# Kernel optimization log

Measured on AMD Instinct MI355X. Metric: run time of the kernel, lower is better.

Reference implementation:

```python
import jax, jax.numpy as jnp
import numpy as np

N_NODES = 50000
N_EDGES = 200000
N_GRAPHS = 1024
D = 24          # node feature dim (fixed by Set2Set(24))
E_FEAT = 8
E_HID = 128


def setup_inputs() -> dict:
    key = jax.random.key(0)
    ks = jax.random.split(key, 20)
    s = 0.1  # weight scale for numerical sanity
    inp = {
        "x": jax.random.normal(ks[0], (N_NODES, D), jnp.float32),
        "edge_attr": jax.random.normal(ks[1], (N_EDGES, E_FEAT), jnp.float32),
        # edge-network MLP: E_FEAT -> E_HID -> D*D
        "w_e1": jax.random.normal(ks[2], (E_FEAT, E_HID), jnp.float32) * s,
        "b_e1": jnp.zeros((E_HID,), jnp.float32),
        "w_e2": jax.random.normal(ks[3], (E_HID, D * D), jnp.float32) * s,
        "b_e2": jnp.zeros((D * D,), jnp.float32),
        # NNConv root weight + bias
        "root": jax.random.normal(ks[4], (D, D), jnp.float32) * s,
        "bias_conv": jnp.zeros((D,), jnp.float32),
        # Set2Set LSTM (input 2D=48, hidden D=24), torch gate order i,f,g,o
        "w_ih": jax.random.normal(ks[5], (4 * D, 2 * D), jnp.float32) * s,
        "w_hh": jax.random.normal(ks[6], (4 * D, D), jnp.float32) * s,
        "b_ih": jnp.zeros((4 * D,), jnp.float32),
        "b_hh": jnp.zeros((4 * D,), jnp.float32),
        # heads
        "w_fc2": jax.random.normal(ks[7], (2 * D, 8), jnp.float32) * s,
        "b_fc2": jnp.zeros((8,), jnp.float32),
        "w_fc3": jax.random.normal(ks[8], (8, 2), jnp.float32) * s,
        "b_fc3": jnp.zeros((2,), jnp.float32),
        "edge_index": jax.random.randint(ks[9], (2, N_EDGES), 0, N_NODES, jnp.int64),
        "batch": jnp.sort(jax.random.randint(ks[10], (N_NODES,), 0, N_GRAPHS, jnp.int64)),
    }
    return inp


def _nnconv(x, edge_attr, edge_index, w_e1, b_e1, w_e2, b_e2, root, bias_conv):
    src, dst = edge_index[0], edge_index[1]
    h = jax.nn.relu(edge_attr @ w_e1 + b_e1)
    w = (h @ w_e2 + b_e2).reshape(-1, D, D)          # [E, D_in, D_out]
    msg = jnp.einsum('ei,eio->eo', x[src], w)         # gather + per-edge matvec
    s = jax.ops.segment_sum(msg, dst, num_segments=N_NODES)
    cnt = jax.ops.segment_sum(jnp.ones((msg.shape[0],), msg.dtype), dst, num_segments=N_NODES)
    agg = s / jnp.maximum(cnt, 1.0)[:, None]          # scatter-mean
    return agg + x @ root + bias_conv


def _set2set(x, batch, w_ih, w_hh, b_ih, b_hh):
    B = N_GRAPHS
    q_star = jnp.zeros((B, 2 * D), x.dtype)
    h = jnp.zeros((B, D), x.dtype)
    c = jnp.zeros((B, D), x.dtype)
    for _ in range(3):  # processing_steps=3 (fixed small loop)
        gates = q_star @ w_ih.T + b_ih + h @ w_hh.T + b_hh
        i, f, g, o = jnp.split(gates, 4, axis=-1)
        c = jax.nn.sigmoid(f) * c + jax.nn.sigmoid(i) * jnp.tanh(g)
        h = jax.nn.sigmoid(o) * jnp.tanh(c)
        q = h                                         # [B, D]
        e = jnp.sum(x * q[batch], axis=-1)            # [N]
        e_max = jax.ops.segment_max(e, batch, num_segments=B)
        e_max = jnp.where(jnp.isfinite(e_max), e_max, 0.0)
        ex = jnp.exp(e - e_max[batch])
        denom = jax.ops.segment_sum(ex, batch, num_segments=B)
        a = ex / jnp.maximum(denom, 1e-16)[batch]     # per-graph softmax
        r = jax.ops.segment_sum(a[:, None] * x, batch, num_segments=B)
        q_star = jnp.concatenate([q, r], axis=-1)
    return q_star


def reference(x, edge_attr, w_e1, b_e1, w_e2, b_e2, root, bias_conv,
              w_ih, w_hh, b_ih, b_hh, w_fc2, b_fc2, w_fc3, b_fc3,
              edge_index, batch):
    x = _nnconv(x, edge_attr, edge_index, w_e1, b_e1, w_e2, b_e2, root, bias_conv)
    x = jax.nn.relu(x)
    x = _nnconv(x, edge_attr, edge_index, w_e1, b_e1, w_e2, b_e2, root, bias_conv)
    q_star = _set2set(x, batch, w_ih, w_hh, b_ih, b_hh)
    out = jax.nn.relu(q_star @ w_fc2 + b_fc2)
    return out @ w_fc3 + b_fc3                        # [B, 2]
```

## Files before the change

kernel.cpp:

```cpp
#include <hip/hip_runtime.h>
#include <math.h>

#define N_NODES 50000
#define N_EDGES 200000
#define N_GRAPHS 1024
#define DIM 24
#define EF 8
#define EH 128
#define DD 576
#define HSTR 136

typedef __attribute__((ext_vector_type(8))) _Float16 f16x8;
typedef __attribute__((ext_vector_type(4))) _Float16 f16x4;
typedef __attribute__((ext_vector_type(2))) _Float16 f16x2;
typedef __attribute__((ext_vector_type(4))) float float4e;
typedef _Float16 f16;

static __device__ __forceinline__ float sigm(float x) { return 1.0f / (1.0f + expf(-x)); }

__global__ void deg_kernel(const int* __restrict__ dst, int* __restrict__ deg) {
    int i = blockIdx.x * blockDim.x + threadIdx.x;
    if (i < N_EDGES) atomicAdd(&deg[dst[i]], 1);
}

__global__ __launch_bounds__(256) void bz_kernel(const float* __restrict__ w2,
                                                 const float* __restrict__ b2,
                                                 f16* __restrict__ Bz) {
    int idx = blockIdx.x * 256 + threadIdx.x;
    if (idx >= 97 * 2 * 64 * 8) return;
    int kk = idx & 7, lane = (idx >> 3) & 63, nt = (idx >> 9) & 1, p = idx >> 10;
    int q = lane >> 4, l16 = lane & 15, n = nt * 16 + l16;
    float v = 0.0f;
    if (p < 96) {
        int si = p / 24, i = p % 24;
        int k = si * 32 + q * 8 + kk;
        if (n < 24) v = w2[(size_t)k * DD + i * 24 + n];
    } else {
        int i2 = q * 8 + kk;
        if (i2 < 24 && n < 24) v = b2[i2 * 24 + n];
    }
    Bz[idx] = (f16)v;
}

__global__ __launch_bounds__(256, 4) void conv_kernel(
    const float* __restrict__ x, const float* __restrict__ ea,
    const float* __restrict__ w1, const float* __restrict__ b1,
    const f16* __restrict__ Bz,
    const int* __restrict__ src, const int* __restrict__ dst,
    float* __restrict__ agg)
{
    __shared__ f16 hs[128 * HSTR];

    const int t  = threadIdx.x;
    const int e0 = blockIdx.x * 128;

    const int lane = t & 63;
    const int wave = t >> 6;
    const int l16  = lane & 15;
    const int quad = lane >> 4;
    const int ebase = e0 + wave * 32;

    f16x2 xa[12], xb[12];
    {
        int ega = ebase + l16;      if (ega >= N_EDGES) ega = N_EDGES - 1;
        int egb = ebase + 16 + l16; if (egb >= N_EDGES) egb = N_EDGES - 1;
        const float* xra = x + (size_t)src[ega] * DIM;
        const float* xrb = x + (size_t)src[egb] * DIM;
        #pragma unroll
        for (int j4 = 0; j4 < 6; ++j4) {
            float4 va = *(const float4*)(xra + j4 * 4);
            float4 vb = *(const float4*)(xrb + j4 * 4);
            xa[j4 * 2]     = (f16x2){(f16)va.x, (f16)va.y};
            xa[j4 * 2 + 1] = (f16x2){(f16)va.z, (f16)va.w};
            xb[j4 * 2]     = (f16x2){(f16)vb.x, (f16)vb.y};
            xb[j4 * 2 + 1] = (f16x2){(f16)vb.z, (f16)vb.w};
        }
    }

    {
        const int s5 = t & 31;
        const int eb = (t >> 5) * 16;
        float wv[EF][4];
        #pragma unroll
        for (int j = 0; j < EF; ++j) {
            float4 v = *(const float4*)(w1 + j * EH + s5 * 4);
            wv[j][0] = v.x; wv[j][1] = v.y; wv[j][2] = v.z; wv[j][3] = v.w;
        }
        float4 bv = *(const float4*)(b1 + s5 * 4);
        const float bvv[4] = {bv.x, bv.y, bv.z, bv.w};
        #pragma unroll
        for (int e = 0; e < 16; ++e) {
            int eg = e0 + eb + e; if (eg >= N_EDGES) eg = N_EDGES - 1;
            const float* ear = ea + (size_t)eg * EF;
            float4 a0 = *(const float4*)ear;
            float4 a1 = *(const float4*)(ear + 4);
            const float av[EF] = {a0.x, a0.y, a0.z, a0.w, a1.x, a1.y, a1.z, a1.w};
            float r[4] = {bvv[0], bvv[1], bvv[2], bvv[3]};
            #pragma unroll
            for (int j = 0; j < EF; ++j)
                #pragma unroll
                for (int c = 0; c < 4; ++c)
                    r[c] = fmaf(av[j], wv[j][c], r[c]);
            f16x4 hq = { (f16)fmaxf(r[0], 0.0f), (f16)fmaxf(r[1], 0.0f),
                         (f16)fmaxf(r[2], 0.0f), (f16)fmaxf(r[3], 0.0f) };
            *(f16x4*)&hs[(eb + e) * HSTR + s5 * 4] = hq;
        }
    }

    const f16x8* bz = (const f16x8*)Bz + lane;
    f16x8 pb0[2], pb1[2];
    pb0[0] = bz[0];   pb1[0] = bz[64];
    pb0[1] = bz[128]; pb1[1] = bz[192];

    __syncthreads();

    float4e a00 = {0.f,0.f,0.f,0.f}, a01 = {0.f,0.f,0.f,0.f};
    float4e a10 = {0.f,0.f,0.f,0.f}, a11 = {0.f,0.f,0.f,0.f};

    #pragma unroll
    for (int si = 0; si < 4; ++si) {
        union { f16x8 v; f16x2 p[4]; } h0u, h1u;
        h0u.v = *(const f16x8*)&hs[(wave * 32 + l16) * HSTR + si * 32 + quad * 8];
        h1u.v = *(const f16x8*)&hs[(wave * 32 + 16 + l16) * HSTR + si * 32 + quad * 8];
        #pragma unroll
        for (int i = 0; i < 24; ++i) {
            const int p = si * 24 + i;
            f16x8 b0 = pb0[p & 1], b1v = pb1[p & 1];
            if (p + 2 <= 96) {
                pb0[p & 1] = bz[(p + 2) * 128];
                pb1[p & 1] = bz[(p + 2) * 128 + 64];
            }
            f16 xea = (i & 1) ? xa[i >> 1][1] : xa[i >> 1][0];
            f16 xeb = (i & 1) ? xb[i >> 1][1] : xb[i >> 1][0];
            f16x2 xa2 = {xea, xea}, xb2 = {xeb, xeb};
            union { f16x8 v; f16x2 p[4]; } a0u, a1u;
            #pragma unroll
            for (int j = 0; j < 4; ++j) {
                a0u.p[j] = h0u.p[j] * xa2;
                a1u.p[j] = h1u.p[j] * xb2;
            }
            a00 = __builtin_amdgcn_mfma_f32_16x16x32_f16(a0u.v, b0,  a00, 0, 0, 0);
            a10 = __builtin_amdgcn_mfma_f32_16x16x32_f16(a1u.v, b0,  a10, 0, 0, 0);
            a01 = __builtin_amdgcn_mfma_f32_16x16x32_f16(a0u.v, b1v, a01, 0, 0, 0);
            a11 = __builtin_amdgcn_mfma_f32_16x16x32_f16(a1u.v, b1v, a11, 0, 0, 0);
            if ((p % 12) == 11) __syncthreads();
        }
    }

    {
        union { f16x8 v; f16x2 p[4]; } a0u, a1u;
        f16x2 z2 = {(f16)0.f, (f16)0.f};
        if (quad == 0)      { a0u.p[0]=xa[0]; a0u.p[1]=xa[1]; a0u.p[2]=xa[2];  a0u.p[3]=xa[3];
                              a1u.p[0]=xb[0]; a1u.p[1]=xb[1]; a1u.p[2]=xb[2];  a1u.p[3]=xb[3];  }
        else if (quad == 1) { a0u.p[0]=xa[4]; a0u.p[1]=xa[5]; a0u.p[2]=xa[6];  a0u.p[3]=xa[7];
                              a1u.p[0]=xb[4]; a1u.p[1]=xb[5]; a1u.p[2]=xb[6];  a1u.p[3]=xb[7];  }
        else if (quad == 2) { a0u.p[0]=xa[8]; a0u.p[1]=xa[9]; a0u.p[2]=xa[10]; a0u.p[3]=xa[11];
                              a1u.p[0]=xb[8]; a1u.p[1]=xb[9]; a1u.p[2]=xb[10]; a1u.p[3]=xb[11]; }
        else                { a0u.p[0]=z2; a0u.p[1]=z2; a0u.p[2]=z2; a0u.p[3]=z2;
                              a1u.p[0]=z2; a1u.p[1]=z2; a1u.p[2]=z2; a1u.p[3]=z2; }
        a00 = __builtin_amdgcn_mfma_f32_16x16x32_f16(a0u.v, pb0[0], a00, 0, 0, 0);
        a10 = __builtin_amdgcn_mfma_f32_16x16x32_f16(a1u.v, pb0[0], a10, 0, 0, 0);
        a01 = __builtin_amdgcn_mfma_f32_16x16x32_f16(a0u.v, pb1[0], a01, 0, 0, 0);
        a11 = __builtin_amdgcn_mfma_f32_16x16x32_f16(a1u.v, pb1[0], a11, 0, 0, 0);
    }

    #pragma unroll
    for (int r = 0; r < 4; ++r) {
        int er = ebase + quad * 4 + r;
        if (er < N_EDGES) {
            int d = dst[er];
            atomicAdd(&agg[(size_t)d * DIM + l16], a00[r]);
            if (l16 < 8) atomicAdd(&agg[(size_t)d * DIM + 16 + l16], a01[r]);
        }
        int er2 = ebase + 16 + quad * 4 + r;
        if (er2 < N_EDGES) {
            int d = dst[er2];
            atomicAdd(&agg[(size_t)d * DIM + l16], a10[r]);
            if (l16 < 8) atomicAdd(&agg[(size_t)d * DIM + 16 + l16], a11[r]);
        }
    }
}

__global__ void combine_kernel(
    const float* __restrict__ x_in, const float* __restrict__ agg,
    const int* __restrict__ deg, const float* __restrict__ root,
    const float* __restrict__ bias, float* __restrict__ x_out, int do_relu)
{
    int t = blockIdx.x * blockDim.x + threadIdx.x;
    if (t >= N_NODES * DIM) return;
    int v = t / DIM, o = t % DIM;
    int dg = deg[v];
    float d = dg > 0 ? (float)dg : 1.0f;
    float a = agg[t] / d + bias[o];
    const float* xr = x_in + (size_t)v * DIM;
    #pragma unroll
    for (int i = 0; i < DIM; ++i) a = fmaf(xr[i], root[i * DIM + o], a);
    x_out[t] = do_relu ? fmaxf(a, 0.0f) : a;
}

__global__ void lstm_kernel(
    const float* __restrict__ q_star, const float* __restrict__ h_in,
    const float* __restrict__ c_in, const float* __restrict__ w_ih,
    const float* __restrict__ w_hh, const float* __restrict__ b_ih,
    const float* __restrict__ b_hh, float* __restrict__ h_out,
    float* __restrict__ c_out)
{
    int t = blockIdx.x * blockDim.x + threadIdx.x;
    if (t >= N_GRAPHS * DIM) return;
    int g = t / DIM, d = t % DIM;
    const float* qs = q_star + (size_t)g * 48;
    const float* hv = h_in + (size_t)g * DIM;
    float gate[4];
    #pragma unroll
    for (int r4 = 0; r4 < 4; ++r4) {
        int r = r4 * DIM + d;
        float a = b_ih[r] + b_hh[r];
        const float* wi = w_ih + (size_t)r * 48;
        const float* wh = w_hh + (size_t)r * DIM;
        for (int j = 0; j < 48; ++j) a = fmaf(qs[j], wi[j], a);
        #pragma unroll
        for (int j = 0; j < DIM; ++j) a = fmaf(hv[j], wh[j], a);
        gate[r4] = a;
    }
    float c = sigm(gate[1]) * c_in[t] + sigm(gate[0]) * tanhf(gate[2]);
    h_out[t] = sigm(gate[3]) * tanhf(c);
    c_out[t] = c;
}

__global__ __launch_bounds__(64) void attn_kernel(
    const float* __restrict__ x, const int* __restrict__ batch,
    const float* __restrict__ h, float* __restrict__ q_star,
    float* __restrict__ e_buf)
{
    const int g = blockIdx.x;
    const int t = threadIdx.x;
    __shared__ int s_lo, s_hi;
    __shared__ float qs[DIM];
    if (t == 0) {
        int lo = 0, hi = N_NODES;
        while (lo < hi) { int m = (lo + hi) >> 1; if (batch[m] < g) lo = m + 1; else hi = m; }
        s_lo = lo;
        int lo2 = lo; hi = N_NODES;
        while (lo2 < hi) { int m = (lo2 + hi) >> 1; if (batch[m] <= g) lo2 = m + 1; else hi = m; }
        s_hi = lo2;
    }
    if (t < DIM) qs[t] = h[(size_t)g * DIM + t];
    __syncthreads();
    const int lo = s_lo, hi = s_hi;

    float mx = -INFINITY;
    for (int n = lo + t; n < hi; n += 64) {
        const float* xr = x + (size_t)n * DIM;
        float e = 0.0f;
        #pragma unroll
        for (int d = 0; d < DIM; ++d) e = fmaf(xr[d], qs[d], e);
        e_buf[n] = e;
        mx = fmaxf(mx, e);
    }
    #pragma unroll
    for (int off = 32; off; off >>= 1) mx = fmaxf(mx, __shfl_xor(mx, off));
    float m = (hi > lo) ? mx : 0.0f;

    float sum = 0.0f;
    for (int n = lo + t; n < hi; n += 64) sum += expf(e_buf[n] - m);
    #pragma unroll
    for (int off = 32; off; off >>= 1) sum += __shfl_xor(sum, off);
    float denom = fmaxf(sum, 1e-16f);

    float r[DIM];
    #pragma unroll
    for (int d = 0; d < DIM; ++d) r[d] = 0.0f;
    for (int n = lo + t; n < hi; n += 64) {
        float a = expf(e_buf[n] - m) / denom;
        const float* xr = x + (size_t)n * DIM;
        #pragma unroll
        for (int d = 0; d < DIM; ++d) r[d] = fmaf(a, xr[d], r[d]);
    }
    #pragma unroll
    for (int d = 0; d < DIM; ++d) {
        #pragma unroll
        for (int off = 32; off; off >>= 1) r[d] += __shfl_xor(r[d], off);
    }
    if (t < DIM) {
        q_star[(size_t)g * 48 + t] = qs[t];
        q_star[(size_t)g * 48 + DIM + t] = r[t];
    }
}

__global__ void head_kernel(
    const float* __restrict__ q_star, const float* __restrict__ w2,
    const float* __restrict__ b2, const float* __restrict__ w3,
    const float* __restrict__ b3, float* __restrict__ out)
{
    int g = blockIdx.x * blockDim.x + threadIdx.x;
    if (g >= N_GRAPHS) return;
    const float* q = q_star + (size_t)g * 48;
    float z[8];
    #pragma unroll
    for (int k = 0; k < 8; ++k) {
        float a = b2[k];
        for (int j = 0; j < 48; ++j) a = fmaf(q[j], w2[j * 8 + k], a);
        z[k] = fmaxf(a, 0.0f);
    }
    #pragma unroll
    for (int c = 0; c < 2; ++c) {
        float a = b3[c];
        #pragma unroll
        for (int k = 0; k < 8; ++k) a = fmaf(z[k], w3[k * 2 + c], a);
        out[(size_t)g * 2 + c] = a;
    }
}

extern "C" void kernel_launch(void* const* d_in, const int* in_sizes, int n_in,
                              void* d_out, int out_size, void* d_ws, size_t ws_size,
                              hipStream_t stream) {
    const float* x      = (const float*)d_in[0];
    const float* ea     = (const float*)d_in[1];
    const float* w_e1   = (const float*)d_in[2];
    const float* b_e1   = (const float*)d_in[3];
    const float* w_e2   = (const float*)d_in[4];
    const float* b_e2   = (const float*)d_in[5];
    const float* root   = (const float*)d_in[6];
    const float* bias_c = (const float*)d_in[7];
    const float* w_ih   = (const float*)d_in[8];
    const float* w_hh   = (const float*)d_in[9];
    const float* b_ih   = (const float*)d_in[10];
    const float* b_hh   = (const float*)d_in[11];
    const float* w_fc2  = (const float*)d_in[12];
    const float* b_fc2  = (const float*)d_in[13];
    const float* w_fc3  = (const float*)d_in[14];
    const float* b_fc3  = (const float*)d_in[15];
    const int*   eidx   = (const int*)d_in[16];
    const int*   batch  = (const int*)d_in[17];
    const int* esrc = eidx;
    const int* edst = eidx + N_EDGES;
    float* out = (float*)d_out;

    char* ws = (char*)d_ws;
    float* agg   = (float*)(ws);
    int*   deg   = (int*)  (ws + 4800000);
    float* qstar = (float*)(ws + 5000000);
    float* h0    = (float*)(ws + 5196608);
    float* c0    = h0 + 24576;
    float* h1    = c0 + 24576;
    float* c1    = h1 + 24576;
    float* ebuf  = (float*)(ws + 5589824);
    float* x1    = (float*)(ws + 5789824);
    float* x2    = (float*)(ws + 10589824);
    f16*   Bz    = (f16*)  (ws + 15389824);

    hipMemsetAsync(ws, 0, 5589824, stream);

    deg_kernel<<<(N_EDGES + 255) / 256, 256, 0, stream>>>(edst, deg);
    bz_kernel<<<(97 * 2 * 64 * 8 + 255) / 256, 256, 0, stream>>>(w_e2, b_e2, Bz);

    conv_kernel<<<(N_EDGES + 127) / 128, 256, 0, stream>>>(x, ea, w_e1, b_e1, Bz, esrc, edst, agg);
    combine_kernel<<<(N_NODES * DIM + 255) / 256, 256, 0, stream>>>(x, agg, deg, root, bias_c, x1, 1);

    hipMemsetAsync(agg, 0, 4800000, stream);
    conv_kernel<<<(N_EDGES + 127) / 128, 256, 0, stream>>>(x1, ea, w_e1, b_e1, Bz, esrc, edst, agg);
    combine_kernel<<<(N_NODES * DIM + 255) / 256, 256, 0, stream>>>(x1, agg, deg, root, bias_c, x2, 0);

    float *hA = h0, *cA = c0, *hB = h1, *cB = c1;
    for (int it = 0; it < 3; ++it) {
        lstm_kernel<<<(N_GRAPHS * DIM + 255) / 256, 256, 0, stream>>>(
            qstar, hA, cA, w_ih, w_hh, b_ih, b_hh, hB, cB);
        attn_kernel<<<N_GRAPHS, 64, 0, stream>>>(x2, batch, hB, qstar, ebuf);
        float* th = hA; hA = hB; hB = th;
        float* tc = cA; cA = cB; cB = tc;
    }

    head_kernel<<<(N_GRAPHS + 255) / 256, 256, 0, stream>>>(qstar, w_fc2, b_fc2, w_fc3, b_fc3, out);
}
```

Measured before the change: 330.2 us.

## Fuse Set2Set LSTM, attention iterations and head into one per-graph kernel

Replaces the three rounds of LSTM and attention launches plus the head kernel with a single kernel in which each block owns one graph and keeps h, c and q_star in shared memory across all iterations. The attention pass becomes a single-pass online softmax with vectorized float4 row loads, so the e buffer and the extra passes over x are gone. This removes seven launches and the global round trips for the intermediates. In exchange the LSTM gate math now runs per block with only 64 threads, and the online rescaling adds extra exp calls when the running max changes.

```diff
diff --git a/kernel.cpp b/kernel.cpp
--- a/kernel.cpp
+++ b/kernel.cpp
@@ -198,44 +198,20 @@
     x_out[t] = do_relu ? fmaxf(a, 0.0f) : a;
 }
 
-__global__ void lstm_kernel(
-    const float* __restrict__ q_star, const float* __restrict__ h_in,
-    const float* __restrict__ c_in, const float* __restrict__ w_ih,
-    const float* __restrict__ w_hh, const float* __restrict__ b_ih,
-    const float* __restrict__ b_hh, float* __restrict__ h_out,
-    float* __restrict__ c_out)
-{
-    int t = blockIdx.x * blockDim.x + threadIdx.x;
-    if (t >= N_GRAPHS * DIM) return;
-    int g = t / DIM, d = t % DIM;
-    const float* qs = q_star + (size_t)g * 48;
-    const float* hv = h_in + (size_t)g * DIM;
-    float gate[4];
-    #pragma unroll
-    for (int r4 = 0; r4 < 4; ++r4) {
-        int r = r4 * DIM + d;
-        float a = b_ih[r] + b_hh[r];
-        const float* wi = w_ih + (size_t)r * 48;
-        const float* wh = w_hh + (size_t)r * DIM;
-        for (int j = 0; j < 48; ++j) a = fmaf(qs[j], wi[j], a);
-        #pragma unroll
-        for (int j = 0; j < DIM; ++j) a = fmaf(hv[j], wh[j], a);
-        gate[r4] = a;
-    }
-    float c = sigm(gate[1]) * c_in[t] + sigm(gate[0]) * tanhf(gate[2]);
-    h_out[t] = sigm(gate[3]) * tanhf(c);
-    c_out[t] = c;
-}
-
-__global__ __launch_bounds__(64) void attn_kernel(
+__global__ __launch_bounds__(64) void s2s_kernel(
     const float* __restrict__ x, const int* __restrict__ batch,
-    const float* __restrict__ h, float* __restrict__ q_star,
-    float* __restrict__ e_buf)
+    const float* __restrict__ w_ih, const float* __restrict__ w_hh,
+    const float* __restrict__ b_ih, const float* __restrict__ b_hh,
+    const float* __restrict__ w_fc2, const float* __restrict__ b_fc2,
+    const float* __restrict__ w_fc3, const float* __restrict__ b_fc3,
+    float* __restrict__ out)
 {
     const int g = blockIdx.x;
     const int t = threadIdx.x;
+    __shared__ float qs[48];
+    __shared__ float hh[24], cc[24], gates[96], zl[8];
     __shared__ int s_lo, s_hi;
-    __shared__ float qs[DIM];
+
     if (t == 0) {
         int lo = 0, hi = N_NODES;
         while (lo < hi) { int m = (lo + hi) >> 1; if (batch[m] < g) lo = m + 1; else hi = m; }
@@ -244,70 +220,86 @@
         while (lo2 < hi) { int m = (lo2 + hi) >> 1; if (batch[m] <= g) lo2 = m + 1; else hi = m; }
         s_hi = lo2;
     }
-    if (t < DIM) qs[t] = h[(size_t)g * DIM + t];
+    if (t < 48) qs[t] = 0.0f;
+    if (t < 24) { hh[t] = 0.0f; cc[t] = 0.0f; }
     __syncthreads();
     const int lo = s_lo, hi = s_hi;
 
-    float mx = -INFINITY;
-    for (int n = lo + t; n < hi; n += 64) {
-        const float* xr = x + (size_t)n * DIM;
-        float e = 0.0f;
-        #pragma unroll
-        for (int d = 0; d < DIM; ++d) e = fmaf(xr[d], qs[d], e);
-        e_buf[n] = e;
-        mx = fmaxf(mx, e);
-    }
-    #pragma unroll
-    for (int off = 32; off; off >>= 1) mx = fmaxf(mx, __shfl_xor(mx, off));
-    float m = (hi > lo) ? mx : 0.0f;
-
-    float sum = 0.0f;
-    for (int n = lo + t; n < hi; n += 64) sum += expf(e_buf[n] - m);
-    #pragma unroll
-    for (int off = 32; off; off >>= 1) sum += __shfl_xor(sum, off);
-    float denom = fmaxf(sum, 1e-16f);
-
-    float r[DIM];
-    #pragma unroll
-    for (int d = 0; d < DIM; ++d) r[d] = 0.0f;
-    for (int n = lo + t; n < hi; n += 64) {
-        float a = expf(e_buf[n] - m) / denom;
-        const float* xr = x + (size_t)n * DIM;
-        #pragma unroll
-        for (int d = 0; d < DIM; ++d) r[d] = fmaf(a, xr[d], r[d]);
-    }
-    #pragma unroll
-    for (int d = 0; d < DIM; ++d) {
-        #pragma unroll
-        for (int off = 32; off; off >>= 1) r[d] += __shfl_xor(r[d], off);
-    }
-    if (t < DIM) {
-        q_star[(size_t)g * 48 + t] = qs[t];
-        q_star[(size_t)g * 48 + DIM + t] = r[t];
-    }
-}
-
-__global__ void head_kernel(
-    const float* __restrict__ q_star, const float* __restrict__ w2,
-    const float* __restrict__ b2, const float* __restrict__ w3,
-    const float* __restrict__ b3, float* __restrict__ out)
-{
-    int g = blockIdx.x * blockDim.x + threadIdx.x;
-    if (g >= N_GRAPHS) return;
-    const float* q = q_star + (size_t)g * 48;
-    float z[8];
-    #pragma unroll
-    for (int k = 0; k < 8; ++k) {
-        float a = b2[k];
-        for (int j = 0; j < 48; ++j) a = fmaf(q[j], w2[j * 8 + k], a);
-        z[k] = fmaxf(a, 0.0f);
-    }
-    #pragma unroll
-    for (int c = 0; c < 2; ++c) {
-        float a = b3[c];
-        #pragma unroll
-        for (int k = 0; k < 8; ++k) a = fmaf(z[k], w3[k * 2 + c], a);
-        out[(size_t)g * 2 + c] = a;
+    for (int it = 0; it < 3; ++it) {
+        for (int rr = t; rr < 96; rr += 64) {
+            float a = b_ih[rr] + b_hh[rr];
+            const float* wi = w_ih + (size_t)rr * 48;
+            const float* wh = w_hh + (size_t)rr * 24;
+            #pragma unroll
+            for (int j = 0; j < 48; ++j) a = fmaf(qs[j], wi[j], a);
+            #pragma unroll
+            for (int j = 0; j < 24; ++j) a = fmaf(hh[j], wh[j], a);
+            gates[rr] = a;
+        }
+        __syncthreads();
+        if (t < 24) {
+            float c = sigm(gates[24 + t]) * cc[t] + sigm(gates[t]) * tanhf(gates[48 + t]);
+            cc[t] = c;
+            float h = sigm(gates[72 + t]) * tanhf(c);
+            hh[t] = h;
+            qs[t] = h;
+        }
+        __syncthreads();
+
+        float m_l = -INFINITY, s_l = 0.0f;
+        float r_l[24];
+        #pragma unroll
+        for (int d = 0; d < 24; ++d) r_l[d] = 0.0f;
+        for (int n = lo + t; n < hi; n += 64) {
+            float xv[24];
+            #pragma unroll
+            for (int j = 0; j < 6; ++j)
+                *(float4*)&xv[j * 4] = ((const float4*)(x + (size_t)n * DIM))[j];
+            float e = 0.0f;
+            #pragma unroll
+            for (int d = 0; d < 24; ++d) e = fmaf(xv[d], qs[d], e);
+            if (e > m_l) {
+                float sc = expf(m_l - e);
+                #pragma unroll
+                for (int d = 0; d < 24; ++d) r_l[d] *= sc;
+                s_l *= sc;
+                m_l = e;
+            }
+            float w = expf(e - m_l);
+            s_l += w;
+            #pragma unroll
+            for (int d = 0; d < 24; ++d) r_l[d] = fmaf(w, xv[d], r_l[d]);
+        }
+        float m = m_l;
+        #pragma unroll
+        for (int off = 32; off; off >>= 1) m = fmaxf(m, __shfl_xor(m, off));
+        float fac = (m_l == -INFINITY) ? 0.0f : expf(m_l - m);
+        float s = s_l * fac;
+        #pragma unroll
+        for (int off = 32; off; off >>= 1) s += __shfl_xor(s, off);
+        float denom = fmaxf(s, 1e-16f);
+        #pragma unroll
+        for (int d = 0; d < 24; ++d) {
+            float rv = r_l[d] * fac;
+            #pragma unroll
+            for (int off = 32; off; off >>= 1) rv += __shfl_xor(rv, off);
+            if (t == d) qs[24 + d] = rv / denom;
+        }
+        __syncthreads();
+    }
+
+    if (t < 8) {
+        float a = b_fc2[t];
+        #pragma unroll
+        for (int j = 0; j < 48; ++j) a = fmaf(qs[j], w_fc2[j * 8 + t], a);
+        zl[t] = fmaxf(a, 0.0f);
+    }
+    __syncthreads();
+    if (t < 2) {
+        float a = b_fc3[t];
+        #pragma unroll
+        for (int k = 0; k < 8; ++k) a = fmaf(zl[k], w_fc3[k * 2 + t], a);
+        out[(size_t)g * 2 + t] = a;
     }
 }
 
@@ -339,17 +331,11 @@
     char* ws = (char*)d_ws;
     float* agg   = (float*)(ws);
     int*   deg   = (int*)  (ws + 4800000);
-    float* qstar = (float*)(ws + 5000000);
-    float* h0    = (float*)(ws + 5196608);
-    float* c0    = h0 + 24576;
-    float* h1    = c0 + 24576;
-    float* c1    = h1 + 24576;
-    float* ebuf  = (float*)(ws + 5589824);
     float* x1    = (float*)(ws + 5789824);
     float* x2    = (float*)(ws + 10589824);
     f16*   Bz    = (f16*)  (ws + 15389824);
 
-    hipMemsetAsync(ws, 0, 5589824, stream);
+    hipMemsetAsync(ws, 0, 5000000, stream);
 
     deg_kernel<<<(N_EDGES + 255) / 256, 256, 0, stream>>>(edst, deg);
     bz_kernel<<<(97 * 2 * 64 * 8 + 255) / 256, 256, 0, stream>>>(w_e2, b_e2, Bz);
@@ -361,14 +347,6 @@
     conv_kernel<<<(N_EDGES + 127) / 128, 256, 0, stream>>>(x1, ea, w_e1, b_e1, Bz, esrc, edst, agg);
     combine_kernel<<<(N_NODES * DIM + 255) / 256, 256, 0, stream>>>(x1, agg, deg, root, bias_c, x2, 0);
 
-    float *hA = h0, *cA = c0, *hB = h1, *cB = c1;
-    for (int it = 0; it < 3; ++it) {
-        lstm_kernel<<<(N_GRAPHS * DIM + 255) / 256, 256, 0, stream>>>(
-            qstar, hA, cA, w_ih, w_hh, b_ih, b_hh, hB, cB);
-        attn_kernel<<<N_GRAPHS, 64, 0, stream>>>(x2, batch, hB, qstar, ebuf);
-        float* th = hA; hA = hB; hB = th;
-        float* tc = cA; cA = cB; cB = tc;
-    }
-
-    head_kernel<<<(N_GRAPHS + 255) / 256, 256, 0, stream>>>(qstar, w_fc2, b_fc2, w_fc3, b_fc3, out);
-}
+    s2s_kernel<<<N_GRAPHS, 64, 0, stream>>>(x2, batch, w_ih, w_hh, b_ih, b_hh,
+                                            w_fc2, b_fc2, w_fc3, b_fc3, out);
+}
```

Result: faster. 301.2 us (-8.8%).
